# Optimization experiments

Measured on AMD Instinct MI355X. Metric: run time of the kernel, lower is better.

The kernel has to match this reference:

```python
import jax, jax.numpy as jnp
import numpy as np

NH, DK, DV, D = 8, 64, 64, 768
DECAY = 0.95
WRITE_STRENGTH = 0.1


def setup_inputs() -> dict:
    key = jax.random.key(0)
    ks = jax.random.split(key, 6)
    s = 0.02  # small init scale for projection weights
    return {
        "x": jax.random.normal(ks[0], (4, 4096, D), dtype=jnp.float32),
        "w_key": jax.random.normal(ks[1], (NH * DK, D), dtype=jnp.float32) * s,
        "w_value": jax.random.normal(ks[2], (NH * DV, D), dtype=jnp.float32) * s,
        "w_query": jax.random.normal(ks[3], (NH * DK, D), dtype=jnp.float32) * s,
        "w_gate": jax.random.normal(ks[4], (NH, D), dtype=jnp.float32) * s,
        "w_out": jax.random.normal(ks[5], (D, NH * DV), dtype=jnp.float32) * s,
    }


def reference(x, w_key, w_value, w_query, w_gate, w_out):
    B, S, _ = x.shape
    # Batched projections (torch Linear: y = x @ W.T)
    k = (x @ w_key.T).reshape(B, S, NH, DK)
    v = (x @ w_value.T).reshape(B, S, NH, DV)
    q = (x @ w_query.T).reshape(B, S, NH, DK)
    gate = jax.nn.sigmoid(x @ w_gate.T)  # (B, S, NH)

    # Writes only use batch element 0 (mirrors k[0], v[0], gate[0] in source)
    k0 = k[0]      # (S, NH, DK)
    v0 = v[0]      # (S, NH, DV)
    g0 = gate[0]   # (S, NH)

    def step(fw, inp):
        q_t, k0_t, v0_t, g0_t = inp
        # Read BEFORE this step's decay+write
        retrieved = jnp.einsum('bhk,hkv->bhv', q_t, fw)  # (B, NH, DV)
        write = (WRITE_STRENGTH * g0_t)[:, None, None] * (k0_t[:, :, None] * v0_t[:, None, :])
        fw_new = DECAY * fw + jax.lax.stop_gradient(write)
        return fw_new, retrieved

    fw0 = jnp.zeros((NH, DK, DV), dtype=x.dtype)
    inputs = (q.transpose(1, 0, 2, 3), k0, v0, g0)  # time-major
    _, retrieved = jax.lax.scan(step, fw0, inputs)   # (S, B, NH, DV)
    retrieved = retrieved.transpose(1, 0, 2, 3).reshape(B, S, NH * DV)
    return x + retrieved @ w_out.T
```

## Files before the change

kernel.cpp:

```cpp
#include <hip/hip_runtime.h>
#include <hip/hip_bf16.h>

typedef __hip_bfloat16 bf16;
typedef __attribute__((ext_vector_type(8))) short   bf16x8;
typedef __attribute__((ext_vector_type(4))) float   f32x4;

#define B_   4
#define S_   4096
#define D_   768
#define NH_  8
#define DK_  64
#define DV_  64
#define CH_  64
#define NCH_ (S_/CH_)
#define DECAY_ 0.95f
#define WSTR_  0.1f

__device__ __forceinline__ float b2f(bf16 v) { return __bfloat162float(v); }
__device__ __forceinline__ bf16  f2b(float v) { return __float2bfloat16(v); }

__device__ __forceinline__ void gl2lds16(const bf16* g, bf16* lds) {
    __builtin_amdgcn_global_load_lds(
        (const __attribute__((address_space(1))) void*)g,
        (__attribute__((address_space(3))) void*)lds, 16, 0, 0);
}

__global__ __launch_bounds__(192) void cast_fused(const float* __restrict__ x,
                                                  bf16* __restrict__ xb,
                                                  const float* __restrict__ wg,
                                                  float* __restrict__ wgt,
                                                  const float* __restrict__ wq,
                                                  const float* __restrict__ wk,
                                                  const float* __restrict__ wv,
                                                  const float* __restrict__ wo,
                                                  bf16* __restrict__ dq, bf16* __restrict__ dk,
                                                  bf16* __restrict__ dv, bf16* __restrict__ dob) {
    const int tid = threadIdx.x;
    if (blockIdx.x >= (B_ * S_)) {
        const int idx = blockIdx.x - B_ * S_;
        const int which = idx >> 9, b = idx & 511;
        const float* src = which == 0 ? wq : which == 1 ? wk : which == 2 ? wv : wo;
        bf16*       dst = which == 0 ? dq : which == 1 ? dk : which == 2 ? dv : dob;
        const int i = (b * 192 + tid) * 4;
        const float4 v = *reinterpret_cast<const float4*>(src + i);
        union { bf16 b4[4]; ushort4 u; } t;
        t.b4[0] = f2b(v.x); t.b4[1] = f2b(v.y); t.b4[2] = f2b(v.z); t.b4[3] = f2b(v.w);
        *reinterpret_cast<ushort4*>(dst + i) = t.u;
        return;
    }
    const int s = blockIdx.x;
    const float4 v = *reinterpret_cast<const float4*>(x + (size_t)s * D_ + tid * 4);
    union { bf16 b4[4]; ushort4 u; } t;
    t.b4[0] = f2b(v.x); t.b4[1] = f2b(v.y); t.b4[2] = f2b(v.z); t.b4[3] = f2b(v.w);
    *reinterpret_cast<ushort4*>(xb + (size_t)s * D_ + tid * 4) = t.u;

    if (s < S_) {
        __shared__ float red[3 * 8];
        float p[8];
        const float* wgp = wg + tid * 4;
        #pragma unroll
        for (int h = 0; h < 8; h++) {
            const float4 wv4 = *reinterpret_cast<const float4*>(wgp + h * D_);
            p[h] = v.x * wv4.x + v.y * wv4.y + v.z * wv4.z + v.w * wv4.w;
        }
        #pragma unroll
        for (int h = 0; h < 8; h++)
            #pragma unroll
            for (int off = 32; off; off >>= 1) p[h] += __shfl_down(p[h], off);
        const int w = tid >> 6, lane = tid & 63;
        if (lane == 0) {
            #pragma unroll
            for (int h = 0; h < 8; h++) red[w * 8 + h] = p[h];
        }
        __syncthreads();
        if (tid < 8) {
            const float sum = red[tid] + red[8 + tid] + red[16 + tid];
            wgt[s * NH_ + tid] = WSTR_ / (1.f + expf(-sum));
        }
    }
}

template<typename TC, int ADDX, int NITER>
__device__ __forceinline__ void gemm_body(bf16* As, bf16* Bs,
                                          const bf16* __restrict__ A,
                                          const bf16* __restrict__ Bm,
                                          const float* __restrict__ X,
                                          TC* __restrict__ C,
                                          int bm, int bn, int K, int N) {
    const int tid = threadIdx.x, lane = tid & 63, w = tid >> 6;
    const int quad = lane >> 4, l16 = lane & 15;
    const int wm = (w >> 1) * 64, wn = (w & 1) * 64;
    const int lrow = lane >> 3;
    const int lcol = ((lane & 7) ^ lrow) * 8;

    f32x4 acc[4][4] = {};

    auto STAGE_A = [&](int it, int buf) {
        const int k0 = it * 64;
        bf16* Ad = As + buf * 8192;
        #pragma unroll
        for (int c = 0; c < 4; c++) {
            const int seg = w * 4 + c;
            const int row = seg * 8 + lrow;
            gl2lds16(A + (size_t)(bm + row) * K + k0 + lcol, &Ad[seg * 512]);
        }
    };
    auto STAGE_B = [&](int it) {
        const int k0 = it * 64;
        #pragma unroll
        for (int c = 0; c < 4; c++) {
            const int seg = w * 4 + c;
            const int row = seg * 8 + lrow;
            gl2lds16(Bm + (size_t)(bn + row) * K + k0 + lcol, &Bs[seg * 512]);
        }
    };

    STAGE_A(0, 0);
    STAGE_B(0);

    for (int it = 0; it < NITER; ++it) {
        const int cur = it & 1;
        if (it + 1 < NITER) {
            STAGE_A(it + 1, cur ^ 1);
            asm volatile("s_waitcnt vmcnt(4)" ::: "memory");
        } else {
            asm volatile("s_waitcnt vmcnt(0)" ::: "memory");
        }
        __builtin_amdgcn_s_barrier();
        asm volatile("" ::: "memory");

        const bf16* Ar = As + cur * 8192;
        bf16x8 af[2][4], bfr[2][4];
        #pragma unroll
        for (int kh = 0; kh < 2; kh++)
            #pragma unroll
            for (int t = 0; t < 4; t++) {
                const int cb = ((kh * 4 + quad) ^ (l16 & 7)) * 8;
                af[kh][t]  = *reinterpret_cast<const bf16x8*>(&Ar[(wm + t * 16 + l16) * 64 + cb]);
                bfr[kh][t] = *reinterpret_cast<const bf16x8*>(&Bs[(wn + t * 16 + l16) * 64 + cb]);
            }
        asm volatile("s_waitcnt lgkmcnt(0)" ::: "memory");
        __builtin_amdgcn_s_barrier();
        if (it + 1 < NITER) STAGE_B(it + 1);

        #pragma unroll
        for (int kh = 0; kh < 2; kh++)
            #pragma unroll
            for (int mt = 0; mt < 4; mt++)
                #pragma unroll
                for (int nt = 0; nt < 4; nt++)
                    acc[mt][nt] = __builtin_amdgcn_mfma_f32_16x16x32_bf16(
                        af[kh][mt], bfr[kh][nt], acc[mt][nt], 0, 0, 0);
    }

    #pragma unroll
    for (int mt = 0; mt < 4; mt++)
        #pragma unroll
        for (int nt = 0; nt < 4; nt++)
            #pragma unroll
            for (int r = 0; r < 4; r++) {
                const int m = bm + wm + mt * 16 + quad * 4 + r;
                const int n = bn + wn + nt * 16 + l16;
                float v = acc[mt][nt][r];
                if (ADDX) v += X[(size_t)m * N + n];
                if (sizeof(TC) == 2) *(bf16*)&C[(size_t)m * N + n] = f2b(v);
                else                 *(float*)&C[(size_t)m * N + n] = v;
            }
}

__global__ __launch_bounds__(256, 3) void proj_fused(const bf16* __restrict__ xb,
                                                  const bf16* __restrict__ wqb,
                                                  const bf16* __restrict__ wkb,
                                                  const bf16* __restrict__ wvb,
                                                  bf16* __restrict__ qbuf,
                                                  bf16* __restrict__ k0buf,
                                                  bf16* __restrict__ v0buf) {
    __shared__ bf16 As[2 * 128 * 64];
    __shared__ bf16 Bs[128 * 64];
    const int id = blockIdx.x;
    const int xcd = id & 7;
    int j = id >> 3;
    const bf16* Bm; bf16* C; int bm, bn;
    if (j < 64) {
        bm = (xcd + ((j >> 2) << 3)) * 128;
        bn = (j & 3) * 128;
        Bm = wqb; C = qbuf;
    } else {
        j -= 64;
        bm = (xcd + ((j >> 3) << 3)) * 128;
        const int b8 = j & 7;
        bn = (b8 & 3) * 128;
        Bm = (b8 < 4) ? wkb : wvb;
        C  = (b8 < 4) ? k0buf : v0buf;
    }
    gemm_body<bf16, 0, 12>(As, Bs, xb, Bm, nullptr, C, bm, bn, D_, 512);
}

__global__ __launch_bounds__(256, 3) void gemm_out(const bf16* __restrict__ retr,
                                                const bf16* __restrict__ wob,
                                                const float* __restrict__ x,
                                                float* __restrict__ out) {
    __shared__ bf16 As[2 * 128 * 64];
    __shared__ bf16 Bs[128 * 64];
    const int gx = gridDim.x, gy = gridDim.y;
    const int L = blockIdx.y * gx + blockIdx.x;
    const int rpx = gy >> 3;
    const int xcd = L & 7;
    const int i   = L >> 3;
    const int by = xcd * rpx + i / gx;
    const int bx = i % gx;
    gemm_body<float, 1, 8>(As, Bs, retr, wob, x, out, by * 128, bx * 128, 512, D_);
}

__global__ __launch_bounds__(256) void chunk_sums(const bf16* __restrict__ k0,
                                                  const bf16* __restrict__ v0,
                                                  const float* __restrict__ wgt,
                                                  bf16* __restrict__ lsumsT) {
    const int n = blockIdx.x, h = blockIdx.y;
    __shared__ float ks[CH_][65];
    __shared__ float vs[CH_][64];
    __shared__ float cw[CH_];
    const int tid = threadIdx.x;
    for (int e = tid; e < CH_ * 64; e += 256) {
        const int r = e >> 6, c = e & 63;
        const int t = n * CH_ + r;
        ks[r][c] = b2f(k0[(size_t)t * (NH_ * DK_) + h * DK_ + c]);
        vs[r][c] = b2f(v0[(size_t)t * (NH_ * DV_) + h * DV_ + c]);
    }
    if (tid < CH_) {
        const int t = n * CH_ + tid;
        cw[tid] = powf(DECAY_, (float)(CH_ - 1 - tid)) * wgt[t * NH_ + h];
    }
    __syncthreads();
    const int j = tid & 63, ig = tid >> 6;
    float acc[16] = {};
    for (int idx = 0; idx < CH_; idx++) {
        const float ck = cw[idx] * ks[idx][j];
        #pragma unroll
        for (int r = 0; r < 16; r++) acc[r] += vs[idx][ig * 16 + r] * ck;
    }
    bf16* outp = lsumsT + ((size_t)(n * NH_ + h)) * (DK_ * DV_);
    #pragma unroll
    for (int r = 0; r < 16; r++) outp[(ig * 16 + r) * 64 + j] = f2b(acc[r]);
}

__device__ __forceinline__ void cvt4(ushort4 u, float f[4]) {
    union { unsigned u; float f; } c;
    c.u = (unsigned)u.x << 16; f[0] = c.f;
    c.u = (unsigned)u.y << 16; f[1] = c.f;
    c.u = (unsigned)u.z << 16; f[2] = c.f;
    c.u = (unsigned)u.w << 16; f[3] = c.f;
}

__global__ __launch_bounds__(256) void chunk_output(const bf16* __restrict__ q,
                                                    const bf16* __restrict__ k0,
                                                    const bf16* __restrict__ v0,
                                                    const float* __restrict__ wgt,
                                                    const bf16* __restrict__ lsumsT,
                                                    bf16* __restrict__ retr) {
    const int n = blockIdx.x, h = blockIdx.y;
    __shared__ bf16 QsAm[4][64 * 64];
    __shared__ bf16 Ks[64 * 64];
    __shared__ bf16 FWT[64 * 64];
    __shared__ bf16 VT[64 * 72];
    __shared__ float dpow[64], winv[64];
    const int tid = threadIdx.x, lane = tid & 63, w = tid >> 6;
    const int quad = lane >> 4, l16 = lane & 15;
    const int t0 = n * CH_;
    const int lrow = lane >> 3;
    const int lcol = ((lane & 7) ^ lrow) * 8;

    #pragma unroll
    for (int seg = 0; seg < 8; seg++) {
        const int row = seg * 8 + lrow;
        gl2lds16(q + ((size_t)(w * S_ + t0 + row)) * 512 + h * 64 + lcol, &QsAm[w][seg * 512]);
    }
    #pragma unroll
    for (int c = 0; c < 2; c++) {
        const int seg = w * 2 + c;
        const int row = seg * 8 + lrow;
        gl2lds16(k0 + ((size_t)(t0 + row)) * 512 + h * 64 + lcol, &Ks[seg * 512]);
    }

    {
        float fwacc[16] = {};
        const float dcp[4] = { 1.0f, 0.0375241f, 1.40806e-3f, 5.28365e-5f };
        #pragma unroll
        for (int jj = 1; jj <= 4; jj++) {
            const int nm = n - jj;
            if (nm < 0) break;
            const ushort* Lp = (const ushort*)(lsumsT + ((size_t)(nm * NH_ + h)) * 4096) + tid * 16;
            #pragma unroll
            for (int u = 0; u < 4; u++) {
                float f[4];
                cvt4(reinterpret_cast<const ushort4*>(Lp)[u], f);
                #pragma unroll
                for (int e = 0; e < 4; e++) fwacc[u * 4 + e] += dcp[jj - 1] * f[e];
            }
        }
        const int frow = tid >> 2;
        #pragma unroll
        for (int half = 0; half < 2; half++) {
            const int cb = (tid & 3) * 2 + half;
            union { bf16 b8v[8]; bf16x8 v; } t;
            #pragma unroll
            for (int e = 0; e < 8; e++) t.b8v[e] = f2b(fwacc[half * 8 + e]);
            *reinterpret_cast<bf16x8*>(&FWT[frow * 64 + (cb ^ (frow & 7)) * 8]) = t.v;
        }
    }
    {
        ushort4 vreg[4];
        const int jb = (tid & 15) * 4;
        const int sb = tid >> 4;
        #pragma unroll
        for (int it = 0; it < 4; it++)
            vreg[it] = *reinterpret_cast<const ushort4*>(
                v0 + ((size_t)(t0 + sb + it * 16)) * 512 + h * 64 + jb);
        ushort* VTu = reinterpret_cast<ushort*>(VT);
        #pragma unroll
        for (int it = 0; it < 4; it++) {
            const int s = sb + it * 16;
            VTu[(jb + 0) * 72 + s] = vreg[it].x;
            VTu[(jb + 1) * 72 + s] = vreg[it].y;
            VTu[(jb + 2) * 72 + s] = vreg[it].z;
            VTu[(jb + 3) * 72 + s] = vreg[it].w;
        }
    }
    if (tid < 64) {
        dpow[tid] = powf(DECAY_, (float)tid);
        winv[tid] = wgt[(t0 + tid) * NH_ + h] * powf(DECAY_, -(float)(tid + 1));
    }
    __syncthreads();

    const int cb0 = ((quad) ^ (l16 & 7)) * 8;
    const int cb1 = ((4 + quad) ^ (l16 & 7)) * 8;
    bf16* Qw = &QsAm[w][0];

    bf16x8 af[4][2];
    #pragma unroll
    for (int mt = 0; mt < 4; mt++) {
        af[mt][0] = *reinterpret_cast<const bf16x8*>(&Qw[(mt * 16 + l16) * 64 + cb0]);
        af[mt][1] = *reinterpret_cast<const bf16x8*>(&Qw[(mt * 16 + l16) * 64 + cb1]);
    }

    f32x4 acc[4][4] = {};
    #pragma unroll
    for (int kh = 0; kh < 2; kh++) {
        bf16x8 bk[4];
        #pragma unroll
        for (int nt = 0; nt < 4; nt++)
            bk[nt] = *reinterpret_cast<const bf16x8*>(
                &Ks[(nt * 16 + l16) * 64 + (kh ? cb1 : cb0)]);
        #pragma unroll
        for (int mt = 0; mt < 4; mt++)
            #pragma unroll
            for (int nt = 0; nt < 4; nt++)
                acc[mt][nt] = __builtin_amdgcn_mfma_f32_16x16x32_bf16(
                    af[mt][kh], bk[nt], acc[mt][nt], 0, 0, 0);
    }

    const float pmt[4] = { 1.0f, 0.4401266694f, 0.1937114891f, 0.0852578070f };
    const f32x4 dpb = *reinterpret_cast<const f32x4*>(&dpow[quad * 4]);
    float winv_l[4];
    #pragma unroll
    for (int nt = 0; nt < 4; nt++) winv_l[nt] = winv[nt * 16 + l16];
    #pragma unroll
    for (int mt = 0; mt < 4; mt++)
        #pragma unroll
        for (int nt = 0; nt < 4; nt++)
            #pragma unroll
            for (int r = 0; r < 4; r++) {
                const int tt = mt * 16 + quad * 4 + r;
                const int s = nt * 16 + l16;
                const float v = (s < tt) ? acc[mt][nt][r] * (dpb[r] * pmt[mt]) * winv_l[nt] : 0.f;
                Qw[tt * 64 + (((s >> 3) ^ (tt & 7)) << 3) + (s & 7)] = f2b(v);
            }

    f32x4 o[4][4] = {};
    #pragma unroll
    for (int kh = 0; kh < 2; kh++) {
        bf16x8 ff[4];
        #pragma unroll
        for (int nt = 0; nt < 4; nt++)
            ff[nt] = *reinterpret_cast<const bf16x8*>(
                &FWT[(nt * 16 + l16) * 64 + (kh ? cb1 : cb0)]);
        #pragma unroll
        for (int mt = 0; mt < 4; mt++)
            #pragma unroll
            for (int nt = 0; nt < 4; nt++)
                o[mt][nt] = __builtin_amdgcn_mfma_f32_16x16x32_bf16(
                    af[mt][kh], ff[nt], o[mt][nt], 0, 0, 0);
    }
    #pragma unroll
    for (int mt = 0; mt < 4; mt++)
        #pragma unroll
        for (int nt = 0; nt < 4; nt++)
            #pragma unroll
            for (int r = 0; r < 4; r++) o[mt][nt][r] *= dpb[r] * pmt[mt];

    #pragma unroll
    for (int kh = 0; kh < 2; kh++) {
        bf16x8 am[4], vf[4];
        #pragma unroll
        for (int mt = 0; mt < 4; mt++)
            am[mt] = *reinterpret_cast<const bf16x8*>(
                &Qw[(mt * 16 + l16) * 64 + (kh ? cb1 : cb0)]);
        #pragma unroll
        for (int nt = 0; nt < 4; nt++)
            vf[nt] = *reinterpret_cast<const bf16x8*>(
                &VT[(nt * 16 + l16) * 72 + kh * 32 + quad * 8]);
        #pragma unroll
        for (int mt = 0; mt < 4; mt++)
            #pragma unroll
            for (int nt = 0; nt < 4; nt++)
                o[mt][nt] = __builtin_amdgcn_mfma_f32_16x16x32_bf16(
                    am[mt], vf[nt], o[mt][nt], 0, 0, 0);
    }

    #pragma unroll
    for (int mt = 0; mt < 4; mt++)
        #pragma unroll
        for (int nt = 0; nt < 4; nt++)
            #pragma unroll
            for (int r = 0; r < 4; r++) {
                const int tt = mt * 16 + quad * 4 + r;
                retr[((size_t)(w * S_ + t0 + tt)) * 512 + h * 64 + nt * 16 + l16] =
                    f2b(o[mt][nt][r]);
            }
}

extern "C" void kernel_launch(void* const* d_in, const int* in_sizes, int n_in,
                              void* d_out, int out_size, void* d_ws, size_t ws_size,
                              hipStream_t stream) {
    const float* x  = (const float*)d_in[0];
    const float* wk = (const float*)d_in[1];
    const float* wv = (const float*)d_in[2];
    const float* wq = (const float*)d_in[3];
    const float* wg = (const float*)d_in[4];
    const float* wo = (const float*)d_in[5];
    float* out = (float*)d_out;

    const size_t MB1 = 1ull << 20;
    char* w = (char*)d_ws;
    bf16*  qbuf    = (bf16*)(w);
    bf16*  k0buf   = (bf16*)(w + 16 * MB1);
    bf16*  v0buf   = (bf16*)(w + 20 * MB1);
    float* wgt     = (float*)(w + 24 * MB1);
    bf16*  wqb     = (bf16*)(w + 24 * MB1 + (128ull<<10));
    bf16*  wkb     = (bf16*)(w + 24 * MB1 + (128ull<<10) + 1*786432);
    bf16*  wvb     = (bf16*)(w + 24 * MB1 + (128ull<<10) + 2*786432);
    bf16*  wob     = (bf16*)(w + 24 * MB1 + (128ull<<10) + 3*786432);
    bf16*  lsumsT  = (bf16*)(w + 28 * MB1);
    bf16*  retr    = (bf16*)(w + 32 * MB1);
    bf16*  xb      = (bf16*)(w + 48 * MB1);

    const int MB = B_ * S_;

    cast_fused<<<MB + 2048, 192, 0, stream>>>(x, xb, wg, wgt,
                                              wq, wk, wv, wo, wqb, wkb, wvb, wob);

    proj_fused<<<768, 256, 0, stream>>>(xb, wqb, wkb, wvb, qbuf, k0buf, v0buf);

    chunk_sums<<<dim3(NCH_, NH_), 256, 0, stream>>>(k0buf, v0buf, wgt, lsumsT);
    chunk_output<<<dim3(NCH_, NH_), 256, 0, stream>>>(qbuf, k0buf, v0buf, wgt, lsumsT, retr);

    gemm_out<<<dim3(D_ / 128, MB / 128), 256, 0, stream>>>(retr, wob, x, out);
}
```

Measured before the change: 185.5 us.

## Alias K and FW tiles in LDS and swizzle VT to raise chunk_output occupancy

The chunk_output kernel now stores the K tile and the decayed fast-weight tile in one shared LDS buffer. The fast-weight tile is written only after the Q·K product is finished, with a barrier on each side of that write. VT drops its 72-column padding in favour of a 64-column XOR swizzle that matches the other tiles, and launch_bounds asks for 3 blocks per CU. This cuts LDS per block so more blocks can be resident. In exchange it adds two barriers, and the fwacc registers stay live across the first MFMA phase, which adds register pressure.

```diff
diff --git a/kernel.cpp b/kernel.cpp
--- a/kernel.cpp
+++ b/kernel.cpp
@@ -23,6 +23,14 @@
     __builtin_amdgcn_global_load_lds(
         (const __attribute__((address_space(1))) void*)g,
         (__attribute__((address_space(3))) void*)lds, 16, 0, 0);
+}
+
+__device__ __forceinline__ void cvt4(ushort4 u, float f[4]) {
+    union { unsigned u; float f; } c;
+    c.u = (unsigned)u.x << 16; f[0] = c.f;
+    c.u = (unsigned)u.y << 16; f[1] = c.f;
+    c.u = (unsigned)u.z << 16; f[2] = c.f;
+    c.u = (unsigned)u.w << 16; f[3] = c.f;
 }
 
 __global__ __launch_bounds__(192) void cast_fused(const float* __restrict__ x,
@@ -244,15 +252,7 @@
     for (int r = 0; r < 16; r++) outp[(ig * 16 + r) * 64 + j] = f2b(acc[r]);
 }
 
-__device__ __forceinline__ void cvt4(ushort4 u, float f[4]) {
-    union { unsigned u; float f; } c;
-    c.u = (unsigned)u.x << 16; f[0] = c.f;
-    c.u = (unsigned)u.y << 16; f[1] = c.f;
-    c.u = (unsigned)u.z << 16; f[2] = c.f;
-    c.u = (unsigned)u.w << 16; f[3] = c.f;
-}
-
-__global__ __launch_bounds__(256) void chunk_output(const bf16* __restrict__ q,
+__global__ __launch_bounds__(256, 3) void chunk_output(const bf16* __restrict__ q,
                                                     const bf16* __restrict__ k0,
                                                     const bf16* __restrict__ v0,
                                                     const float* __restrict__ wgt,
@@ -260,9 +260,8 @@
                                                     bf16* __restrict__ retr) {
     const int n = blockIdx.x, h = blockIdx.y;
     __shared__ bf16 QsAm[4][64 * 64];
-    __shared__ bf16 Ks[64 * 64];
-    __shared__ bf16 FWT[64 * 64];
-    __shared__ bf16 VT[64 * 72];
+    __shared__ bf16 KsFWT[64 * 64];
+    __shared__ bf16 VT[64 * 64];
     __shared__ float dpow[64], winv[64];
     const int tid = threadIdx.x, lane = tid & 63, w = tid >> 6;
     const int quad = lane >> 4, l16 = lane & 15;
@@ -279,11 +278,10 @@
     for (int c = 0; c < 2; c++) {
         const int seg = w * 2 + c;
         const int row = seg * 8 + lrow;
-        gl2lds16(k0 + ((size_t)(t0 + row)) * 512 + h * 64 + lcol, &Ks[seg * 512]);
-    }
-
+        gl2lds16(k0 + ((size_t)(t0 + row)) * 512 + h * 64 + lcol, &KsFWT[seg * 512]);
+    }
+    float fwacc[16] = {};
     {
-        float fwacc[16] = {};
         const float dcp[4] = { 1.0f, 0.0375241f, 1.40806e-3f, 5.28365e-5f };
         #pragma unroll
         for (int jj = 1; jj <= 4; jj++) {
@@ -298,15 +296,6 @@
                 for (int e = 0; e < 4; e++) fwacc[u * 4 + e] += dcp[jj - 1] * f[e];
             }
         }
-        const int frow = tid >> 2;
-        #pragma unroll
-        for (int half = 0; half < 2; half++) {
-            const int cb = (tid & 3) * 2 + half;
-            union { bf16 b8v[8]; bf16x8 v; } t;
-            #pragma unroll
-            for (int e = 0; e < 8; e++) t.b8v[e] = f2b(fwacc[half * 8 + e]);
-            *reinterpret_cast<bf16x8*>(&FWT[frow * 64 + (cb ^ (frow & 7)) * 8]) = t.v;
-        }
     }
     {
         ushort4 vreg[4];
@@ -320,10 +309,13 @@
         #pragma unroll
         for (int it = 0; it < 4; it++) {
             const int s = sb + it * 16;
-            VTu[(jb + 0) * 72 + s] = vreg[it].x;
-            VTu[(jb + 1) * 72 + s] = vreg[it].y;
-            VTu[(jb + 2) * 72 + s] = vreg[it].z;
-            VTu[(jb + 3) * 72 + s] = vreg[it].w;
+            #pragma unroll
+            for (int c = 0; c < 4; c++) {
+                const int v = jb + c;
+                const ushort val = c == 0 ? vreg[it].x : c == 1 ? vreg[it].y
+                                 : c == 2 ? vreg[it].z : vreg[it].w;
+                VTu[v * 64 + (((s >> 3) ^ (v & 7)) << 3) + (s & 7)] = val;
+            }
         }
     }
     if (tid < 64) {
@@ -350,7 +342,7 @@
         #pragma unroll
         for (int nt = 0; nt < 4; nt++)
             bk[nt] = *reinterpret_cast<const bf16x8*>(
-                &Ks[(nt * 16 + l16) * 64 + (kh ? cb1 : cb0)]);
+                &KsFWT[(nt * 16 + l16) * 64 + (kh ? cb1 : cb0)]);
         #pragma unroll
         for (int mt = 0; mt < 4; mt++)
             #pragma unroll
@@ -375,6 +367,19 @@
                 const float v = (s < tt) ? acc[mt][nt][r] * (dpb[r] * pmt[mt]) * winv_l[nt] : 0.f;
                 Qw[tt * 64 + (((s >> 3) ^ (tt & 7)) << 3) + (s & 7)] = f2b(v);
             }
+    __syncthreads();
+    {
+        const int frow = tid >> 2;
+        #pragma unroll
+        for (int half = 0; half < 2; half++) {
+            const int cb = (tid & 3) * 2 + half;
+            union { bf16 b8v[8]; bf16x8 v; } t;
+            #pragma unroll
+            for (int e = 0; e < 8; e++) t.b8v[e] = f2b(fwacc[half * 8 + e]);
+            *reinterpret_cast<bf16x8*>(&KsFWT[frow * 64 + (cb ^ (frow & 7)) * 8]) = t.v;
+        }
+    }
+    __syncthreads();
 
     f32x4 o[4][4] = {};
     #pragma unroll
@@ -383,7 +388,7 @@
         #pragma unroll
         for (int nt = 0; nt < 4; nt++)
             ff[nt] = *reinterpret_cast<const bf16x8*>(
-                &FWT[(nt * 16 + l16) * 64 + (kh ? cb1 : cb0)]);
+                &KsFWT[(nt * 16 + l16) * 64 + (kh ? cb1 : cb0)]);
         #pragma unroll
         for (int mt = 0; mt < 4; mt++)
             #pragma unroll
@@ -408,7 +413,7 @@
         #pragma unroll
         for (int nt = 0; nt < 4; nt++)
             vf[nt] = *reinterpret_cast<const bf16x8*>(
-                &VT[(nt * 16 + l16) * 72 + kh * 32 + quad * 8]);
+                &VT[(nt * 16 + l16) * 64 + (kh ? cb1 : cb0)]);
         #pragma unroll
         for (int mt = 0; mt < 4; mt++)
             #pragma unroll
```

After: 184.9 us. About the same (-0.3%).
